# Kernel tuning notes

Measured on AMD Instinct MI355X. Metric: run time of the kernel, lower is better.

Reference implementation:

```python
import jax, jax.numpy as jnp
import numpy as np

B, LAT, ADIM, NACT, H = 131072, 64, 16, 9, 128

def setup_inputs() -> dict:
    key = jax.random.key(0)
    ks = jax.random.split(key, 24)
    p = lambda k, shp: (jax.random.normal(k, shp, dtype=jnp.float32) * 0.05)
    return {
        "z_t": jax.random.normal(ks[0], (B, LAT), dtype=jnp.float32),
        "action": jax.random.randint(ks[1], (B,), 0, NACT),
        "hidden": jnp.zeros((1, B, H), dtype=jnp.float32),
        "embed": p(ks[2], (NACT, ADIM)),
        "fuse_W": p(ks[3], (H, LAT + ADIM)), "fuse_b": p(ks[4], (H,)),
        "W_ih": p(ks[5], (3 * H, H)), "W_hh": p(ks[6], (3 * H, H)),
        "b_ih": p(ks[7], (3 * H,)), "b_hh": p(ks[8], (3 * H,)),
        "ns_W1": p(ks[9], (H, H)), "ns_b1": p(ks[10], (H,)),
        "ns_W2": p(ks[11], (LAT, H)), "ns_b2": p(ks[12], (LAT,)),
        "rw_W1": p(ks[13], (H // 2, H)), "rw_b1": p(ks[14], (H // 2,)),
        "rw_W2": p(ks[15], (1, H // 2)), "rw_b2": p(ks[16], (1,)),
        "dn_W1": p(ks[17], (H // 2, H)), "dn_b1": p(ks[18], (H // 2,)),
        "dn_W2": p(ks[19], (1, H // 2)), "dn_b2": p(ks[20], (1,)),
    }

def _mlp2(x, W1, b1, W2, b2):
    return jax.nn.relu(x @ W1.T + b1) @ W2.T + b2

def reference(z_t, action, hidden, embed, fuse_W, fuse_b, W_ih, W_hh, b_ih, b_hh,
              ns_W1, ns_b1, ns_W2, ns_b2, rw_W1, rw_b1, rw_W2, rw_b2,
              dn_W1, dn_b1, dn_W2, dn_b2):
    a_emb = embed[action]                                  # [B, ADIM]
    fused = jnp.concatenate([z_t, a_emb], axis=-1)         # [B, LAT+ADIM]
    x = jax.nn.relu(fused @ fuse_W.T + fuse_b)             # [B, H]
    h0 = hidden[0]                                         # [B, H]
    gi = x @ W_ih.T + b_ih                                 # [B, 3H]
    gh = h0 @ W_hh.T + b_hh                                # [B, 3H]
    Hd = x.shape[-1]
    r = jax.nn.sigmoid(gi[:, :Hd] + gh[:, :Hd])
    zg = jax.nn.sigmoid(gi[:, Hd:2 * Hd] + gh[:, Hd:2 * Hd])
    n = jnp.tanh(gi[:, 2 * Hd:] + r * gh[:, 2 * Hd:])
    h_new = (1.0 - zg) * n + zg * h0                       # [B, H]
    out = h_new
    z_next = _mlp2(out, ns_W1, ns_b1, ns_W2, ns_b2)        # [B, LAT]
    reward = _mlp2(out, rw_W1, rw_b1, rw_W2, rw_b2)        # [B, 1]
    done_logit = _mlp2(out, dn_W1, dn_b1, dn_W2, dn_b2)    # [B, 1]
    return (z_next, reward, done_logit, h_new[None])
```

## Files before the change

### kernel.cpp

```cpp
#include <hip/hip_runtime.h>
#include <hip/hip_bf16.h>
#include <cstddef>
#include <cstdint>

#define BATCH 131072
#define HOFF ((size_t)BATCH * 66)

typedef __attribute__((ext_vector_type(8))) short short8;
typedef __attribute__((ext_vector_type(4))) short short4v;
typedef __attribute__((ext_vector_type(4))) float f32x4;

typedef const __attribute__((address_space(1))) unsigned int* gas_t;
typedef __attribute__((address_space(3))) unsigned int* las_t;

#define WS_GRU   13312
#define WS_HEAD  (13312 + 16*6656)
#define WS_ELEMS (WS_HEAD + 10*4352)

#define G_BASE   13312
#define STR_BASE 66560

#define MFMA(a,b,c) __builtin_amdgcn_mfma_f32_16x16x32_bf16((a),(b),(c),0,0,0)

__device__ __forceinline__ short f2bf(float x) {
    __hip_bfloat16 b = __float2bfloat16(x);
    return __builtin_bit_cast(short, b);
}
__device__ __forceinline__ float bf2f(short s) {
    unsigned u = ((unsigned)(unsigned short)s) << 16;
    return __builtin_bit_cast(float, u);
}
__device__ __forceinline__ float fsigmoid(float x) { return __builtin_amdgcn_rcpf(1.0f + __expf(-x)); }
__device__ __forceinline__ float ftanh(float x)    { return 1.0f - 2.0f * __builtin_amdgcn_rcpf(1.0f + __expf(2.0f * x)); }

__device__ __forceinline__ short8 packbf(f32x4 a, f32x4 b) {
    short8 r;
    r[0]=f2bf(a[0]); r[1]=f2bf(a[1]); r[2]=f2bf(a[2]); r[3]=f2bf(a[3]);
    r[4]=f2bf(b[0]); r[5]=f2bf(b[1]); r[6]=f2bf(b[2]); r[7]=f2bf(b[3]);
    return r;
}

template<int NCH>
__device__ __forceinline__ void stage_lds(const short* __restrict__ src, short* dst, int t) {
    constexpr int NP = (NCH + 511) / 512;
    #pragma unroll
    for (int k = 0; k < NP; ++k) {
        int c = t + 512 * k;
        if ((NCH % 512 == 0) || c < NCH)
            __builtin_amdgcn_global_load_lds((gas_t)(const void*)(src + (size_t)c * 8),
                                             (las_t)(void*)(dst + (size_t)c * 8), 16, 0, 0);
    }
}

extern "C" __global__ void prep_weights(const float* __restrict__ fuse_W,
                                        const float* __restrict__ W_ih, const float* __restrict__ W_hh,
                                        const float* __restrict__ ns_W1, const float* __restrict__ ns_W2,
                                        const float* __restrict__ rw_W1, const float* __restrict__ dn_W1,
                                        short* __restrict__ ws) {
    int i = blockIdx.x * 256 + threadIdx.x;
    if (i >= WS_ELEMS) return;
    float v = 0.f;
    if (i < WS_GRU) {
        int j = i / 104, k = i % 104;
        if (k < 80) v = fuse_W[j*80 + k];
    } else if (i < WS_HEAD) {
        int g = (i - WS_GRU) / 6656, e = (i - WS_GRU) % 6656;
        int r = e / 136, k = e % 136;
        if (r < 48 && k < 128) {
            int j = g >> 1;
            const float* W = (g & 1) ? W_hh : W_ih;
            int gate = r >> 4, rr = r & 15;
            v = W[(size_t)(gate*128 + j*16 + rr)*128 + k];
        }
    } else {
        int h = (i - WS_HEAD) / 4352, e = (i - WS_HEAD) % 4352;
        int r = e / 136, k = e % 136;
        if (k < 128) {
            const float* W; int rb;
            if (h < 4)      { W = ns_W1; rb = h*32; }
            else if (h < 6) { W = ns_W2; rb = (h-4)*32; }
            else if (h < 8) { W = rw_W1; rb = (h-6)*32; }
            else            { W = dn_W1; rb = (h-8)*32; }
            v = W[(size_t)(rb + r)*128 + k];
        }
    }
    ws[i] = f2bf(v);
}

#define HEAD_GEMM(FRAG, BIAS, Q, UBASE, RELU) do {                                          \
    _Pragma("unroll") for (int sub = 0; sub < 2; ++sub) {                                   \
        float bb = (BIAS)[(Q)*32 + sub*16 + lo];                                            \
        f32x4 a0 = zz4, a1 = zz4;                                                           \
        _Pragma("unroll") for (int kt = 0; kt < 4; ++kt) {                                  \
            short8 Bf = *(const short8*)&smem[(UBASE) + (sub*16+lo)*136 + kt*32 + hi*8];    \
            a0 = MFMA((FRAG)[0][kt], Bf, a0); a1 = MFMA((FRAG)[1][kt], Bf, a1); }           \
        _Pragma("unroll") for (int e = 0; e < 4; ++e) {                                     \
            float v0 = a0[e] + bb, v1 = a1[e] + bb;                                         \
            if (RELU) { v0 = fmaxf(v0, 0.f); v1 = fmaxf(v1, 0.f); }                         \
            S[(4*hi+e)*40 + sub*16 + lo]      = f2bf(v0);                                   \
            S[(16+4*hi+e)*40 + sub*16 + lo]   = f2bf(v1); }                                 \
    } } while (0)

#define AFRAG_READ(DST, Q) do {                                        \
    (DST)[0][Q] = *(const short8*)&S[lo*40 + hi*8];                    \
    (DST)[1][Q] = *(const short8*)&S[(16+lo)*40 + hi*8]; } while (0)

#define GRU_J(JJ) do {                                                                      \
    const int ihB = G_BASE + (2*((JJ)&3))*6656;                                             \
    const int hhB = ihB + 6656;                                                             \
    const int j0 = (JJ)*16;                                                                 \
    const float bir = b_ih[j0+lo], biz = b_ih[128+j0+lo], bin = b_ih[256+j0+lo];            \
    const float bhr = b_hh[j0+lo], bhz = b_hh[128+j0+lo], bhn = b_hh[256+j0+lo];            \
    f32x4 accI[3][2], accH[3][2];                                                           \
    _Pragma("unroll") for (int g = 0; g < 3; ++g) {                                         \
        accI[g][0]=zz4; accI[g][1]=zz4; accH[g][0]=zz4; accH[g][1]=zz4;                     \
        _Pragma("unroll") for (int kt = 0; kt < 4; ++kt) {                                  \
            short8 Bi = *(const short8*)&smem[ihB + (g*16+lo)*136 + kt*32 + hi*8];          \
            accI[g][0] = MFMA(xa[0][kt], Bi, accI[g][0]);                                   \
            accI[g][1] = MFMA(xa[1][kt], Bi, accI[g][1]);                                   \
            short8 Bh = *(const short8*)&smem[hhB + (g*16+lo)*136 + kt*32 + hi*8];          \
            accH[g][0] = MFMA(ha[0][kt], Bh, accH[g][0]);                                   \
            accH[g][1] = MFMA(ha[1][kt], Bh, accH[g][1]);                                   \
        }                                                                                   \
    }                                                                                       \
    _Pragma("unroll") for (int rt = 0; rt < 2; ++rt)                                        \
    _Pragma("unroll") for (int p = 0; p < 2; ++p) {                                         \
        unsigned hp = h0d[JJ][rt][p];                                                       \
        float h0a = bf2f((short)(hp & 0xffffu));                                            \
        float h0b = bf2f((short)(hp >> 16));                                                \
        int e = 2*p;                                                                        \
        { float rg = fsigmoid(accI[0][rt][e] + bir + accH[0][rt][e] + bhr);                 \
          float zg = fsigmoid(accI[1][rt][e] + biz + accH[1][rt][e] + bhz);                 \
          float ng = ftanh(accI[2][rt][e] + bin + rg*(accH[2][rt][e] + bhn));               \
          S[(rt*16 + 4*hi + e)*40 + ((JJ)&1)*16 + lo] = f2bf((1.f-zg)*ng + zg*h0a); }       \
        { float rg = fsigmoid(accI[0][rt][e+1] + bir + accH[0][rt][e+1] + bhr);             \
          float zg = fsigmoid(accI[1][rt][e+1] + biz + accH[1][rt][e+1] + bhz);             \
          float ng = ftanh(accI[2][rt][e+1] + bin + rg*(accH[2][rt][e+1] + bhn));           \
          S[(rt*16 + 4*hi + e+1)*40 + ((JJ)&1)*16 + lo] = f2bf((1.f-zg)*ng + zg*h0b); }     \
    }                                                                                       \
} while (0)

extern "C" __global__ __launch_bounds__(512, 1)
void gru_mfma(const float* __restrict__ z_t, const int* __restrict__ action,
              const float* __restrict__ hidden, const float* __restrict__ embed,
              const float* __restrict__ fuse_b,
              const float* __restrict__ b_ih, const float* __restrict__ b_hh,
              const float* __restrict__ ns_b1, const float* __restrict__ ns_b2,
              const float* __restrict__ rw_b1, const float* __restrict__ rw_W2, const float* __restrict__ rw_b2,
              const float* __restrict__ dn_b1, const float* __restrict__ dn_W2, const float* __restrict__ dn_b2,
              const short* __restrict__ ws, float* out)
{
    __shared__ __align__(16) short smem[76800];

    const int t    = threadIdx.x;
    const int lane = t & 63;
    const int w    = t >> 6;
    const int lo   = lane & 15;
    const int hi   = lane >> 4;
    const int R    = blockIdx.x * 256 + w * 32;
    short* const S = &smem[STR_BASE + w * 1280];

    const f32x4 zz4 = {0.f, 0.f, 0.f, 0.f};

    auto store_hnew_strip = [&](int kt) {
        #pragma unroll
        for (int v = 0; v < 4; ++v) {
            int idx = v*64 + lane;
            int r = idx >> 3, c = (idx & 7) * 4;
            short4v s = *(const short4v*)&S[r*40 + c];
            f32x4 f = { bf2f(s[0]), bf2f(s[1]), bf2f(s[2]), bf2f(s[3]) };
            *(f32x4*)&out[HOFF + (size_t)(R + r)*128 + kt*32 + c] = f;
        }
    };
    auto store_z_strip = [&](int q) {
        #pragma unroll
        for (int v = 0; v < 4; ++v) {
            int idx = v*64 + lane;
            int r = idx >> 3, c = (idx & 7) * 4;
            short4v s = *(const short4v*)&S[r*40 + c];
            f32x4 f = { bf2f(s[0]), bf2f(s[1]), bf2f(s[2]), bf2f(s[3]) };
            *(f32x4*)&out[(size_t)(R + r)*64 + q*32 + c] = f;
        }
    };
    auto hpartial = [&](const float* W2, float acc) -> float {
        int rr = lane & 31;
        #pragma unroll
        for (int kk = 0; kk < 32; kk += 8) {
            short8 s = *(const short8*)&S[rr*40 + kk];
            f32x4 w0 = *(const f32x4*)&W2[kk];
            f32x4 w1 = *(const f32x4*)&W2[kk+4];
            acc += bf2f(s[0])*w0[0] + bf2f(s[1])*w0[1] + bf2f(s[2])*w0[2] + bf2f(s[3])*w0[3]
                 + bf2f(s[4])*w1[0] + bf2f(s[5])*w1[1] + bf2f(s[6])*w1[2] + bf2f(s[7])*w1[3];
        }
        return acc;
    };

    stage_lds<1664>(ws, &smem[0], t);
    stage_lds<6656>(ws + WS_GRU, &smem[G_BASE], t);

    short8 fa[2][3];
    short8 ha[2][4];
    #pragma unroll
    for (int rt = 0; rt < 2; ++rt) {
        const int row = R + rt*16 + lo;
        #pragma unroll
        for (int kt = 0; kt < 2; ++kt) {
            f32x4 p0 = *(const f32x4*)&z_t[(size_t)row*64 + kt*32 + hi*8];
            f32x4 p1 = *(const f32x4*)&z_t[(size_t)row*64 + kt*32 + hi*8 + 4];
            fa[rt][kt] = packbf(p0, p1);
        }
        if (hi < 2) {
            int a = action[row];
            f32x4 e0 = *(const f32x4*)&embed[a*16 + hi*8];
            f32x4 e1 = *(const f32x4*)&embed[a*16 + hi*8 + 4];
            fa[rt][2] = packbf(e0, e1);
        } else {
            short8 z8 = {0,0,0,0,0,0,0,0};
            fa[rt][2] = z8;
        }
        #pragma unroll
        for (int kt = 0; kt < 4; ++kt) {
            f32x4 p0 = *(const f32x4*)&hidden[(size_t)row*128 + kt*32 + hi*8];
            f32x4 p1 = *(const f32x4*)&hidden[(size_t)row*128 + kt*32 + hi*8 + 4];
            ha[rt][kt] = packbf(p0, p1);
        }
    }
    float fbv[8];
    #pragma unroll
    for (int ct = 0; ct < 8; ++ct) fbv[ct] = fuse_b[ct*16 + lo];

    unsigned h0d[8][2][2];
    #pragma unroll
    for (int kt = 0; kt < 4; ++kt) {
        *(short8*)&S[lo*40 + hi*8]        = ha[0][kt];
        *(short8*)&S[(16 + lo)*40 + hi*8] = ha[1][kt];
        #pragma unroll
        for (int c = 0; c < 2; ++c) {
            int j = 2*kt + c;
            #pragma unroll
            for (int rt = 0; rt < 2; ++rt)
                #pragma unroll
                for (int p = 0; p < 2; ++p) {
                    unsigned a = (unsigned short)S[(rt*16 + 4*hi + 2*p    )*40 + c*16 + lo];
                    unsigned b = (unsigned short)S[(rt*16 + 4*hi + 2*p + 1)*40 + c*16 + lo];
                    h0d[j][rt][p] = a | (b << 16);
                }
        }
    }
    __syncthreads();

    short8 xa[2][4];
    #pragma unroll
    for (int kt = 0; kt < 4; ++kt) {
        #pragma unroll
        for (int c = 0; c < 2; ++c) {
            int ct = kt*2 + c;
            f32x4 a0 = zz4, a1 = zz4;
            #pragma unroll
            for (int fk = 0; fk < 3; ++fk) {
                short8 B = *(const short8*)&smem[(ct*16 + lo)*104 + fk*32 + hi*8];
                a0 = MFMA(fa[0][fk], B, a0);
                a1 = MFMA(fa[1][fk], B, a1);
            }
            #pragma unroll
            for (int e = 0; e < 4; ++e) {
                S[(4*hi + e)*40 + c*16 + lo]      = f2bf(fmaxf(a0[e] + fbv[ct], 0.f));
                S[(16 + 4*hi + e)*40 + c*16 + lo] = f2bf(fmaxf(a1[e] + fbv[ct], 0.f));
            }
        }
        AFRAG_READ(xa, kt);
    }

    short8 hfa[2][4];
    GRU_J(0);
    GRU_J(1); AFRAG_READ(hfa, 0); store_hnew_strip(0);
    GRU_J(2);
    GRU_J(3); AFRAG_READ(hfa, 1); store_hnew_strip(1);

    __syncthreads();
    stage_lds<6656>(ws + WS_GRU + 8*6656, &smem[G_BASE], t);
    __syncthreads();

    GRU_J(4);
    GRU_J(5); AFRAG_READ(hfa, 2); store_hnew_strip(2);
    GRU_J(6);
    GRU_J(7); AFRAG_READ(hfa, 3); store_hnew_strip(3);

    __syncthreads();
    stage_lds<5440>(ws + WS_HEAD, &smem[G_BASE], t);
    __syncthreads();

    short8 ta[2][4];
    HEAD_GEMM(hfa, ns_b1, 0, G_BASE + 0*4352, true);  AFRAG_READ(ta, 0);
    HEAD_GEMM(hfa, ns_b1, 1, G_BASE + 1*4352, true);  AFRAG_READ(ta, 1);
    HEAD_GEMM(hfa, ns_b1, 2, G_BASE + 2*4352, true);  AFRAG_READ(ta, 2);
    HEAD_GEMM(hfa, ns_b1, 3, G_BASE + 3*4352, true);  AFRAG_READ(ta, 3);
    HEAD_GEMM(ta,  ns_b2, 0, G_BASE + 4*4352, false); store_z_strip(0);
    HEAD_GEMM(ta,  ns_b2, 1, G_BASE + 5*4352, false); store_z_strip(1);

    float racc = rw_b2[0];
    HEAD_GEMM(hfa, rw_b1, 0, G_BASE + 6*4352, true);  racc = hpartial(rw_W2, racc);
    HEAD_GEMM(hfa, rw_b1, 1, G_BASE + 7*4352, true);  racc = hpartial(rw_W2 + 32, racc);
    if (lane < 32) out[(size_t)BATCH*64 + R + (lane & 31)] = racc;

    float dacc = dn_b2[0];
    HEAD_GEMM(hfa, dn_b1, 0, G_BASE + 8*4352, true);  dacc = hpartial(dn_W2, dacc);
    HEAD_GEMM(hfa, dn_b1, 1, G_BASE + 9*4352, true);  dacc = hpartial(dn_W2 + 32, dacc);
    if (lane < 32) out[(size_t)BATCH*65 + R + (lane & 31)] = dacc;
}

extern "C" void kernel_launch(void* const* d_in, const int* in_sizes, int n_in,
                              void* d_out, int out_size, void* d_ws, size_t ws_size,
                              hipStream_t stream) {
    const float* z_t    = (const float*)d_in[0];
    const int*   action = (const int*)  d_in[1];
    const float* hidden = (const float*)d_in[2];
    const float* embed  = (const float*)d_in[3];
    const float* fuse_W = (const float*)d_in[4];
    const float* fuse_b = (const float*)d_in[5];
    const float* W_ih   = (const float*)d_in[6];
    const float* W_hh   = (const float*)d_in[7];
    const float* b_ih   = (const float*)d_in[8];
    const float* b_hh   = (const float*)d_in[9];
    const float* ns_W1  = (const float*)d_in[10];
    const float* ns_b1  = (const float*)d_in[11];
    const float* ns_W2  = (const float*)d_in[12];
    const float* ns_b2  = (const float*)d_in[13];
    const float* rw_W1  = (const float*)d_in[14];
    const float* rw_b1  = (const float*)d_in[15];
    const float* rw_W2  = (const float*)d_in[16];
    const float* rw_b2  = (const float*)d_in[17];
    const float* dn_W1  = (const float*)d_in[18];
    const float* dn_b1  = (const float*)d_in[19];
    const float* dn_W2  = (const float*)d_in[20];
    const float* dn_b2  = (const float*)d_in[21];
    float* out = (float*)d_out;
    short* ws  = (short*)d_ws;

    hipLaunchKernelGGL(prep_weights, dim3((WS_ELEMS + 255) / 256), dim3(256), 0, stream,
                       fuse_W, W_ih, W_hh, ns_W1, ns_W2, rw_W1, dn_W1, ws);

    hipLaunchKernelGGL(gru_mfma, dim3(BATCH / 256), dim3(512), 0, stream,
                       z_t, action, hidden, embed,
                       fuse_b, b_ih, b_hh, ns_b1, ns_b2,
                       rw_b1, rw_W2, rw_b2, dn_b1, dn_W2, dn_b2,
                       ws, out);
}
```

Baseline: 83.72 us.

## Switch all GEMMs from 16x16x32 to 32x32x16 bf16 MFMA with relaid weights

```diff
diff --git a/kernel.cpp b/kernel.cpp
--- a/kernel.cpp
+++ b/kernel.cpp
@@ -9,18 +9,20 @@
 typedef __attribute__((ext_vector_type(8))) short short8;
 typedef __attribute__((ext_vector_type(4))) short short4v;
 typedef __attribute__((ext_vector_type(4))) float f32x4;
+typedef __attribute__((ext_vector_type(16))) float f32x16;
 
 typedef const __attribute__((address_space(1))) unsigned int* gas_t;
 typedef __attribute__((address_space(3))) unsigned int* las_t;
 
-#define WS_GRU   13312
-#define WS_HEAD  (13312 + 16*6656)
-#define WS_ELEMS (WS_HEAD + 10*4352)
-
-#define G_BASE   13312
-#define STR_BASE 66560
-
-#define MFMA(a,b,c) __builtin_amdgcn_mfma_f32_16x16x32_bf16((a),(b),(c),0,0,0)
+#define WS_GRU    13312
+#define WS_GUNIT  26112
+#define WS_HEAD   117760
+#define WS_ELEMS  161280
+
+#define G_BASE    13312
+#define STR_BASE  65536
+
+#define MFMA32(a,b,c) __builtin_amdgcn_mfma_f32_32x32x16_bf16((a),(b),(c),0,0,0)
 
 __device__ __forceinline__ short f2bf(float x) {
     __hip_bfloat16 b = __float2bfloat16(x);
@@ -64,16 +66,18 @@
         int j = i / 104, k = i % 104;
         if (k < 80) v = fuse_W[j*80 + k];
     } else if (i < WS_HEAD) {
-        int g = (i - WS_GRU) / 6656, e = (i - WS_GRU) % 6656;
-        int r = e / 136, k = e % 136;
-        if (r < 48 && k < 128) {
-            int j = g >> 1;
-            const float* W = (g & 1) ? W_hh : W_ih;
-            int gate = r >> 4, rr = r & 15;
-            v = W[(size_t)(gate*128 + j*16 + rr)*128 + k];
+        int rel = i - WS_GRU;
+        int u2 = rel / WS_GUNIT, e = rel % WS_GUNIT;
+        int rb = e / 136, k = e % 136;
+        if (k < 128) {
+            int gp = rb >> 5, r = rb & 31;
+            int g = gp >> 1, p = gp & 1;
+            const float* W = p ? W_hh : W_ih;
+            v = W[(size_t)(g*128 + u2*32 + r)*128 + k];
         }
     } else {
-        int h = (i - WS_HEAD) / 4352, e = (i - WS_HEAD) % 4352;
+        int rel = i - WS_HEAD;
+        int h = rel / 4352, e = rel % 4352;
         int r = e / 136, k = e % 136;
         if (k < 128) {
             const float* W; int rb;
@@ -87,57 +91,54 @@
     ws[i] = f2bf(v);
 }
 
-#define HEAD_GEMM(FRAG, BIAS, Q, UBASE, RELU) do {                                          \
-    _Pragma("unroll") for (int sub = 0; sub < 2; ++sub) {                                   \
-        float bb = (BIAS)[(Q)*32 + sub*16 + lo];                                            \
-        f32x4 a0 = zz4, a1 = zz4;                                                           \
-        _Pragma("unroll") for (int kt = 0; kt < 4; ++kt) {                                  \
-            short8 Bf = *(const short8*)&smem[(UBASE) + (sub*16+lo)*136 + kt*32 + hi*8];    \
-            a0 = MFMA((FRAG)[0][kt], Bf, a0); a1 = MFMA((FRAG)[1][kt], Bf, a1); }           \
-        _Pragma("unroll") for (int e = 0; e < 4; ++e) {                                     \
-            float v0 = a0[e] + bb, v1 = a1[e] + bb;                                         \
-            if (RELU) { v0 = fmaxf(v0, 0.f); v1 = fmaxf(v1, 0.f); }                         \
-            S[(4*hi+e)*40 + sub*16 + lo]      = f2bf(v0);                                   \
-            S[(16+4*hi+e)*40 + sub*16 + lo]   = f2bf(v1); }                                 \
-    } } while (0)
-
-#define AFRAG_READ(DST, Q) do {                                        \
-    (DST)[0][Q] = *(const short8*)&S[lo*40 + hi*8];                    \
-    (DST)[1][Q] = *(const short8*)&S[(16+lo)*40 + hi*8]; } while (0)
-
-#define GRU_J(JJ) do {                                                                      \
-    const int ihB = G_BASE + (2*((JJ)&3))*6656;                                             \
-    const int hhB = ihB + 6656;                                                             \
-    const int j0 = (JJ)*16;                                                                 \
-    const float bir = b_ih[j0+lo], biz = b_ih[128+j0+lo], bin = b_ih[256+j0+lo];            \
-    const float bhr = b_hh[j0+lo], bhz = b_hh[128+j0+lo], bhn = b_hh[256+j0+lo];            \
-    f32x4 accI[3][2], accH[3][2];                                                           \
-    _Pragma("unroll") for (int g = 0; g < 3; ++g) {                                         \
-        accI[g][0]=zz4; accI[g][1]=zz4; accH[g][0]=zz4; accH[g][1]=zz4;                     \
-        _Pragma("unroll") for (int kt = 0; kt < 4; ++kt) {                                  \
-            short8 Bi = *(const short8*)&smem[ihB + (g*16+lo)*136 + kt*32 + hi*8];          \
-            accI[g][0] = MFMA(xa[0][kt], Bi, accI[g][0]);                                   \
-            accI[g][1] = MFMA(xa[1][kt], Bi, accI[g][1]);                                   \
-            short8 Bh = *(const short8*)&smem[hhB + (g*16+lo)*136 + kt*32 + hi*8];          \
-            accH[g][0] = MFMA(ha[0][kt], Bh, accH[g][0]);                                   \
-            accH[g][1] = MFMA(ha[1][kt], Bh, accH[g][1]);                                   \
-        }                                                                                   \
-    }                                                                                       \
-    _Pragma("unroll") for (int rt = 0; rt < 2; ++rt)                                        \
-    _Pragma("unroll") for (int p = 0; p < 2; ++p) {                                         \
-        unsigned hp = h0d[JJ][rt][p];                                                       \
-        float h0a = bf2f((short)(hp & 0xffffu));                                            \
-        float h0b = bf2f((short)(hp >> 16));                                                \
-        int e = 2*p;                                                                        \
-        { float rg = fsigmoid(accI[0][rt][e] + bir + accH[0][rt][e] + bhr);                 \
-          float zg = fsigmoid(accI[1][rt][e] + biz + accH[1][rt][e] + bhz);                 \
-          float ng = ftanh(accI[2][rt][e] + bin + rg*(accH[2][rt][e] + bhn));               \
-          S[(rt*16 + 4*hi + e)*40 + ((JJ)&1)*16 + lo] = f2bf((1.f-zg)*ng + zg*h0a); }       \
-        { float rg = fsigmoid(accI[0][rt][e+1] + bir + accH[0][rt][e+1] + bhr);             \
-          float zg = fsigmoid(accI[1][rt][e+1] + biz + accH[1][rt][e+1] + bhz);             \
-          float ng = ftanh(accI[2][rt][e+1] + bin + rg*(accH[2][rt][e+1] + bhn));           \
-          S[(rt*16 + 4*hi + e+1)*40 + ((JJ)&1)*16 + lo] = f2bf((1.f-zg)*ng + zg*h0b); }     \
-    }                                                                                       \
+#define GRU_J2(U, J2) do {                                                                 \
+    const int ub = G_BASE + (U)*WS_GUNIT;                                                  \
+    const int cb = (J2)*32 + ln;                                                           \
+    const float br  = b_ih[cb]       + b_hh[cb];                                           \
+    const float bz  = b_ih[128 + cb] + b_hh[128 + cb];                                     \
+    const float bin = b_ih[256 + cb];                                                      \
+    const float bhn = b_hh[256 + cb];                                                      \
+    f32x16 ar = zz16, az = zz16, ain = zz16, ahn = zz16;                                   \
+    _Pragma("unroll") for (int kf = 0; kf < 8; ++kf) {                                     \
+        const int ko = kf*16 + hb8;                                                        \
+        short8 B0 = *(const short8*)&smem[ub + (0*32 + ln)*136 + ko];                      \
+        ar  = MFMA32(xa[kf], B0, ar);                                                      \
+        short8 B1 = *(const short8*)&smem[ub + (1*32 + ln)*136 + ko];                      \
+        ar  = MFMA32(ha[kf], B1, ar);                                                      \
+        short8 B2 = *(const short8*)&smem[ub + (2*32 + ln)*136 + ko];                      \
+        az  = MFMA32(xa[kf], B2, az);                                                      \
+        short8 B3 = *(const short8*)&smem[ub + (3*32 + ln)*136 + ko];                      \
+        az  = MFMA32(ha[kf], B3, az);                                                      \
+        short8 B4 = *(const short8*)&smem[ub + (4*32 + ln)*136 + ko];                      \
+        ain = MFMA32(xa[kf], B4, ain);                                                     \
+        short8 B5 = *(const short8*)&smem[ub + (5*32 + ln)*136 + ko];                      \
+        ahn = MFMA32(ha[kf], B5, ahn);                                                     \
+    }                                                                                      \
+    _Pragma("unroll") for (int p = 0; p < 8; ++p) {                                        \
+        unsigned hp = h0d[J2][p];                                                          \
+        _Pragma("unroll") for (int q = 0; q < 2; ++q) {                                    \
+            const int reg = 2*p + q;                                                       \
+            float h0v = bf2f((short)(q ? (hp >> 16) : (hp & 0xffffu)));                    \
+            float rg = fsigmoid(ar[reg] + br);                                             \
+            float zg = fsigmoid(az[reg] + bz);                                             \
+            float ng = ftanh(ain[reg] + bin + rg*(ahn[reg] + bhn));                        \
+            S[((reg&3) + 8*(reg>>2) + hr4)*40 + ln] = f2bf((1.f - zg)*ng + zg*h0v);        \
+        }                                                                                  \
+    }                                                                                      \
+} while (0)
+
+#define HEAD32(FRAG, BIASEXPR, HU, RELU) do {                                              \
+    f32x16 a = zz16;                                                                       \
+    _Pragma("unroll") for (int kf = 0; kf < 8; ++kf) {                                     \
+        short8 B = *(const short8*)&smem[G_BASE + (HU)*4352 + ln*136 + kf*16 + hb8];       \
+        a = MFMA32((FRAG)[kf], B, a);                                                      \
+    }                                                                                      \
+    const float bb = (BIASEXPR);                                                           \
+    _Pragma("unroll") for (int reg = 0; reg < 16; ++reg) {                                 \
+        float v = a[reg] + bb;                                                             \
+        if (RELU) v = fmaxf(v, 0.f);                                                       \
+        S[((reg&3) + 8*(reg>>2) + hr4)*40 + ln] = f2bf(v);                                 \
+    }                                                                                      \
 } while (0)
 
 extern "C" __global__ __launch_bounds__(512, 1)
@@ -150,29 +151,30 @@
               const float* __restrict__ dn_b1, const float* __restrict__ dn_W2, const float* __restrict__ dn_b2,
               const short* __restrict__ ws, float* out)
 {
-    __shared__ __align__(16) short smem[76800];
+    __shared__ __align__(16) short smem[75776];
 
     const int t    = threadIdx.x;
     const int lane = t & 63;
     const int w    = t >> 6;
-    const int lo   = lane & 15;
-    const int hi   = lane >> 4;
+    const int ln   = lane & 31;
+    const int hb8  = (lane >> 5) * 8;
+    const int hr4  = (lane >> 5) * 4;
     const int R    = blockIdx.x * 256 + w * 32;
     short* const S = &smem[STR_BASE + w * 1280];
 
-    const f32x4 zz4 = {0.f, 0.f, 0.f, 0.f};
-
-    auto store_hnew_strip = [&](int kt) {
+    const f32x16 zz16 = {0,0,0,0,0,0,0,0,0,0,0,0,0,0,0,0};
+
+    auto store_hnew = [&](int j2) {
         #pragma unroll
         for (int v = 0; v < 4; ++v) {
             int idx = v*64 + lane;
             int r = idx >> 3, c = (idx & 7) * 4;
             short4v s = *(const short4v*)&S[r*40 + c];
             f32x4 f = { bf2f(s[0]), bf2f(s[1]), bf2f(s[2]), bf2f(s[3]) };
-            *(f32x4*)&out[HOFF + (size_t)(R + r)*128 + kt*32 + c] = f;
+            *(f32x4*)&out[HOFF + (size_t)(R + r)*128 + j2*32 + c] = f;
         }
     };
-    auto store_z_strip = [&](int q) {
+    auto store_z = [&](int q) {
         #pragma unroll
         for (int v = 0; v < 4; ++v) {
             int idx = v*64 + lane;
@@ -196,117 +198,115 @@
     };
 
     stage_lds<1664>(ws, &smem[0], t);
-    stage_lds<6656>(ws + WS_GRU, &smem[G_BASE], t);
-
-    short8 fa[2][3];
-    short8 ha[2][4];
+    stage_lds<6528>(ws + WS_GRU, &smem[G_BASE], t);
+
+    short8 fa[5];
+    short8 ha[8];
+    {
+        const int row = R + ln;
+        #pragma unroll
+        for (int kf = 0; kf < 4; ++kf) {
+            f32x4 p0 = *(const f32x4*)&z_t[(size_t)row*64 + kf*16 + hb8];
+            f32x4 p1 = *(const f32x4*)&z_t[(size_t)row*64 + kf*16 + hb8 + 4];
+            fa[kf] = packbf(p0, p1);
+        }
+        int a = action[row];
+        f32x4 e0 = *(const f32x4*)&embed[a*16 + hb8];
+        f32x4 e1 = *(const f32x4*)&embed[a*16 + hb8 + 4];
+        fa[4] = packbf(e0, e1);
+        #pragma unroll
+        for (int kf = 0; kf < 8; ++kf) {
+            f32x4 p0 = *(const f32x4*)&hidden[(size_t)row*128 + kf*16 + hb8];
+            f32x4 p1 = *(const f32x4*)&hidden[(size_t)row*128 + kf*16 + hb8 + 4];
+            ha[kf] = packbf(p0, p1);
+        }
+    }
+
+    unsigned h0d[4][8];
     #pragma unroll
-    for (int rt = 0; rt < 2; ++rt) {
-        const int row = R + rt*16 + lo;
-        #pragma unroll
-        for (int kt = 0; kt < 2; ++kt) {
-            f32x4 p0 = *(const f32x4*)&z_t[(size_t)row*64 + kt*32 + hi*8];
-            f32x4 p1 = *(const f32x4*)&z_t[(size_t)row*64 + kt*32 + hi*8 + 4];
-            fa[rt][kt] = packbf(p0, p1);
-        }
-        if (hi < 2) {
-            int a = action[row];
-            f32x4 e0 = *(const f32x4*)&embed[a*16 + hi*8];
-            f32x4 e1 = *(const f32x4*)&embed[a*16 + hi*8 + 4];
-            fa[rt][2] = packbf(e0, e1);
-        } else {
-            short8 z8 = {0,0,0,0,0,0,0,0};
-            fa[rt][2] = z8;
-        }
-        #pragma unroll
-        for (int kt = 0; kt < 4; ++kt) {
-            f32x4 p0 = *(const f32x4*)&hidden[(size_t)row*128 + kt*32 + hi*8];
-            f32x4 p1 = *(const f32x4*)&hidden[(size_t)row*128 + kt*32 + hi*8 + 4];
-            ha[rt][kt] = packbf(p0, p1);
-        }
-    }
-    float fbv[8];
+    for (int n = 0; n < 4; ++n) {
+        *(short8*)&S[ln*40 + hb8]      = ha[2*n];
+        *(short8*)&S[ln*40 + 16 + hb8] = ha[2*n+1];
+        #pragma unroll
+        for (int p = 0; p < 8; ++p) {
+            const int r0 = 2*p, r1 = 2*p + 1;
+            unsigned a = (unsigned short)S[((r0&3) + 8*(r0>>2) + hr4)*40 + ln];
+            unsigned b = (unsigned short)S[((r1&3) + 8*(r1>>2) + hr4)*40 + ln];
+            h0d[n][p] = a | (b << 16);
+        }
+    }
+    __syncthreads();
+
+    short8 xa[8];
     #pragma unroll
-    for (int ct = 0; ct < 8; ++ct) fbv[ct] = fuse_b[ct*16 + lo];
-
-    unsigned h0d[8][2][2];
-    #pragma unroll
-    for (int kt = 0; kt < 4; ++kt) {
-        *(short8*)&S[lo*40 + hi*8]        = ha[0][kt];
-        *(short8*)&S[(16 + lo)*40 + hi*8] = ha[1][kt];
-        #pragma unroll
-        for (int c = 0; c < 2; ++c) {
-            int j = 2*kt + c;
-            #pragma unroll
-            for (int rt = 0; rt < 2; ++rt)
-                #pragma unroll
-                for (int p = 0; p < 2; ++p) {
-                    unsigned a = (unsigned short)S[(rt*16 + 4*hi + 2*p    )*40 + c*16 + lo];
-                    unsigned b = (unsigned short)S[(rt*16 + 4*hi + 2*p + 1)*40 + c*16 + lo];
-                    h0d[j][rt][p] = a | (b << 16);
-                }
-        }
-    }
-    __syncthreads();
-
-    short8 xa[2][4];
-    #pragma unroll
-    for (int kt = 0; kt < 4; ++kt) {
-        #pragma unroll
-        for (int c = 0; c < 2; ++c) {
-            int ct = kt*2 + c;
-            f32x4 a0 = zz4, a1 = zz4;
-            #pragma unroll
-            for (int fk = 0; fk < 3; ++fk) {
-                short8 B = *(const short8*)&smem[(ct*16 + lo)*104 + fk*32 + hi*8];
-                a0 = MFMA(fa[0][fk], B, a0);
-                a1 = MFMA(fa[1][fk], B, a1);
-            }
-            #pragma unroll
-            for (int e = 0; e < 4; ++e) {
-                S[(4*hi + e)*40 + c*16 + lo]      = f2bf(fmaxf(a0[e] + fbv[ct], 0.f));
-                S[(16 + 4*hi + e)*40 + c*16 + lo] = f2bf(fmaxf(a1[e] + fbv[ct], 0.f));
-            }
-        }
-        AFRAG_READ(xa, kt);
-    }
-
-    short8 hfa[2][4];
-    GRU_J(0);
-    GRU_J(1); AFRAG_READ(hfa, 0); store_hnew_strip(0);
-    GRU_J(2);
-    GRU_J(3); AFRAG_READ(hfa, 1); store_hnew_strip(1);
-
-    __syncthreads();
-    stage_lds<6656>(ws + WS_GRU + 8*6656, &smem[G_BASE], t);
-    __syncthreads();
-
-    GRU_J(4);
-    GRU_J(5); AFRAG_READ(hfa, 2); store_hnew_strip(2);
-    GRU_J(6);
-    GRU_J(7); AFRAG_READ(hfa, 3); store_hnew_strip(3);
+    for (int n = 0; n < 4; ++n) {
+        f32x16 a = zz16;
+        #pragma unroll
+        for (int kf = 0; kf < 5; ++kf) {
+            short8 B = *(const short8*)&smem[(n*32 + ln)*104 + kf*16 + hb8];
+            a = MFMA32(fa[kf], B, a);
+        }
+        float fb = fuse_b[n*32 + ln];
+        #pragma unroll
+        for (int reg = 0; reg < 16; ++reg)
+            S[((reg&3) + 8*(reg>>2) + hr4)*40 + ln] = f2bf(fmaxf(a[reg] + fb, 0.f));
+        xa[2*n]   = *(const short8*)&S[ln*40 + hb8];
+        xa[2*n+1] = *(const short8*)&S[ln*40 + 16 + hb8];
+    }
+
+    short8 hfa[8];
+    GRU_J2(0, 0);
+    hfa[0] = *(const short8*)&S[ln*40 + hb8];
+    hfa[1] = *(const short8*)&S[ln*40 + 16 + hb8];
+    store_hnew(0);
+    GRU_J2(1, 1);
+    hfa[2] = *(const short8*)&S[ln*40 + hb8];
+    hfa[3] = *(const short8*)&S[ln*40 + 16 + hb8];
+    store_hnew(1);
+
+    __syncthreads();
+    stage_lds<6528>(ws + WS_GRU + 2*WS_GUNIT, &smem[G_BASE], t);
+    __syncthreads();
+
+    GRU_J2(0, 2);
+    hfa[4] = *(const short8*)&S[ln*40 + hb8];
+    hfa[5] = *(const short8*)&S[ln*40 + 16 + hb8];
+    store_hnew(2);
+    GRU_J2(1, 3);
+    hfa[6] = *(const short8*)&S[ln*40 + hb8];
+    hfa[7] = *(const short8*)&S[ln*40 + 16 + hb8];
+    store_hnew(3);
 
     __syncthreads();
     stage_lds<5440>(ws + WS_HEAD, &smem[G_BASE], t);
     __syncthreads();
 
-    short8 ta[2][4];
-    HEAD_GEMM(hfa, ns_b1, 0, G_BASE + 0*4352, true);  AFRAG_READ(ta, 0);
-    HEAD_GEMM(hfa, ns_b1, 1, G_BASE + 1*4352, true);  AFRAG_READ(ta, 1);
-    HEAD_GEMM(hfa, ns_b1, 2, G_BASE + 2*4352, true);  AFRAG_READ(ta, 2);
-    HEAD_GEMM(hfa, ns_b1, 3, G_BASE + 3*4352, true);  AFRAG_READ(ta, 3);
-    HEAD_GEMM(ta,  ns_b2, 0, G_BASE + 4*4352, false); store_z_strip(0);
-    HEAD_GEMM(ta,  ns_b2, 1, G_BASE + 5*4352, false); store_z_strip(1);
+    short8 ta[8];
+    HEAD32(hfa, ns_b1[ln],      0, true);
+    ta[0] = *(const short8*)&S[ln*40 + hb8];
+    ta[1] = *(const short8*)&S[ln*40 + 16 + hb8];
+    HEAD32(hfa, ns_b1[32 + ln], 1, true);
+    ta[2] = *(const short8*)&S[ln*40 + hb8];
+    ta[3] = *(const short8*)&S[ln*40 + 16 + hb8];
+    HEAD32(hfa, ns_b1[64 + ln], 2, true);
+    ta[4] = *(const short8*)&S[ln*40 + hb8];
+    ta[5] = *(const short8*)&S[ln*40 + 16 + hb8];
+    HEAD32(hfa, ns_b1[96 + ln], 3, true);
+    ta[6] = *(const short8*)&S[ln*40 + hb8];
+    ta[7] = *(const short8*)&S[ln*40 + 16 + hb8];
+
+    HEAD32(ta, ns_b2[ln],      4, false); store_z(0);
+    HEAD32(ta, ns_b2[32 + ln], 5, false); store_z(1);
 
     float racc = rw_b2[0];
-    HEAD_GEMM(hfa, rw_b1, 0, G_BASE + 6*4352, true);  racc = hpartial(rw_W2, racc);
-    HEAD_GEMM(hfa, rw_b1, 1, G_BASE + 7*4352, true);  racc = hpartial(rw_W2 + 32, racc);
-    if (lane < 32) out[(size_t)BATCH*64 + R + (lane & 31)] = racc;
+    HEAD32(hfa, rw_b1[ln],      6, true); racc = hpartial(rw_W2, racc);
+    HEAD32(hfa, rw_b1[32 + ln], 7, true); racc = hpartial(rw_W2 + 32, racc);
+    if (lane < 32) out[(size_t)BATCH*64 + R + ln] = racc;
 
     float dacc = dn_b2[0];
-    HEAD_GEMM(hfa, dn_b1, 0, G_BASE + 8*4352, true);  dacc = hpartial(dn_W2, dacc);
-    HEAD_GEMM(hfa, dn_b1, 1, G_BASE + 9*4352, true);  dacc = hpartial(dn_W2 + 32, dacc);
-    if (lane < 32) out[(size_t)BATCH*65 + R + (lane & 31)] = dacc;
+    HEAD32(hfa, dn_b1[ln],      8, true); dacc = hpartial(dn_W2, dacc);
+    HEAD32(hfa, dn_b1[32 + ln], 9, true); dacc = hpartial(dn_W2 + 32, dacc);
+    if (lane < 32) out[(size_t)BATCH*65 + R + ln] = dacc;
 }
 
 extern "C" void kernel_launch(void* const* d_in, const int* in_sizes, int n_in,
```

Result: slower. 92.29 us (+10.2%).
